# Kernel tuning notes

Measured on AMD Instinct MI355X. Metric: run time of the kernel, lower is better.

The kernel has to match this reference:

```python
import jax, jax.numpy as jnp
import numpy as np

B, L, H = 4, 1024, 8192
NH, HD = 64, 128
PD = HD // 2  # 64, rope-style positional dim
QL = HD * 4 * 3  # 1536, Q latent dim
KVL = HD * 4     # 512, KV latent dim


def setup_inputs() -> dict:
    key = jax.random.key(0)
    ks = jax.random.split(key, 18)
    w = lambda k, i, o: (jax.random.normal(k, (i, o), jnp.float32) * (1.0 / np.sqrt(i))).astype(jnp.float32)
    b = lambda k, o: jnp.zeros((o,), jnp.float32)
    return {
        'x': jax.random.normal(ks[0], (B, L, H), jnp.float32),
        'W_dq': w(ks[1], H, QL),   'b_dq': b(ks[2], QL),
        'W_dkv': w(ks[3], H, KVL), 'b_dkv': b(ks[4], KVL),
        'W_uq': w(ks[5], QL, H),   'b_uq': b(ks[6], H),
        'W_uk': w(ks[7], KVL, H),  'b_uk': b(ks[8], H),
        'W_uv': w(ks[9], KVL, H),  'b_uv': b(ks[10], H),
        'W_pq': w(ks[11], QL, NH * PD), 'b_pq': b(ks[12], NH * PD),
        'W_pk': w(ks[13], H, PD),  'b_pk': b(ks[14], PD),
        'W_o': w(ks[15], H, H),    'b_o': b(ks[16], H),
    }


def reference(x, W_dq, b_dq, W_dkv, b_dkv, W_uq, b_uq, W_uk, b_uk,
              W_uv, b_uv, W_pq, b_pq, W_pk, b_pk, W_o, b_o):
    Bb, Ll, Hh = x.shape
    # low-rank latents
    Q_lat = x @ W_dq + b_dq          # (B, L, 1536)
    KV_lat = x @ W_dkv + b_dkv       # (B, L, 512)
    # up-projections
    Q_c = (Q_lat @ W_uq + b_uq).reshape(Bb, Ll, NH, HD)
    Q_r = (Q_lat @ W_pq + b_pq).reshape(Bb, Ll, NH, PD)
    Q = jnp.concatenate([Q_c, Q_r], axis=-1)            # (B, L, NH, 192)
    K_c = (KV_lat @ W_uk + b_uk).reshape(Bb, Ll, NH, HD)
    K_r = x @ W_pk + b_pk                                # (B, L, 64), shared across heads
    K_r = jnp.broadcast_to(K_r[:, :, None, :], (Bb, Ll, NH, PD))
    K = jnp.concatenate([K_c, K_r], axis=-1)             # (B, L, NH, 192)
    V = (KV_lat @ W_uv + b_uv).reshape(Bb, Ll, NH, HD)   # (B, L, NH, 128)
    # attention with mismatched Q/K (192) vs V (128) head dims; scale by sqrt(128)
    scores = jnp.einsum('bqhd,bkhd->bhqk', Q, K) / np.float32(np.sqrt(HD))
    causal = jnp.tril(jnp.ones((Ll, Ll), bool))
    scores = jnp.where(causal, scores, jnp.float32(-jnp.inf))
    attn = jax.nn.softmax(scores, axis=-1)               # dropout = identity (eval)
    out = jnp.einsum('bhqk,bkhd->bqhd', attn, V).reshape(Bb, Ll, Hh)
    return out @ W_o + b_o
```

## Files before the change

### kernel.cpp

```cpp
#include <hip/hip_runtime.h>
#include <cstdint>

typedef unsigned short u16;
typedef __attribute__((ext_vector_type(8))) short bf16x8;
typedef __attribute__((ext_vector_type(4))) float f32x4;
typedef __attribute__((ext_vector_type(4))) unsigned short u16x4;

__device__ __forceinline__ u16 f2b(float f) {
  union { float f; uint32_t u; } v; v.f = f;
  uint32_t r = v.u + 0x7FFFu + ((v.u >> 16) & 1u);
  return (u16)(r >> 16);
}

__device__ __forceinline__ void gload_lds16(const void* g, void* l) {
  __builtin_amdgcn_global_load_lds((const __attribute__((address_space(1))) void*)g,
                                   (__attribute__((address_space(3))) void*)l, 16, 0, 0);
}

__device__ __forceinline__ void barrier_raw() {
  __builtin_amdgcn_sched_barrier(0);
  asm volatile("" ::: "memory");
  __builtin_amdgcn_s_barrier();
  asm volatile("" ::: "memory");
  __builtin_amdgcn_sched_barrier(0);
}
__device__ __forceinline__ void wait_vm8() {
  asm volatile("s_waitcnt vmcnt(8)" ::: "memory");
  __builtin_amdgcn_sched_barrier(0);
}

__global__ __launch_bounds__(256) void cvt_bf16(const float* __restrict__ in,
                                                u16* __restrict__ out, long n) {
  long i = ((long)blockIdx.x * 256 + threadIdx.x) * 4;
  if (i >= n) return;
  f32x4 v = *(const f32x4*)(in + i);
  u16x4 o;
#pragma unroll
  for (int k = 0; k < 4; k++) o[k] = f2b(v[k]);
  *(u16x4*)(out + i) = o;
}

__global__ __launch_bounds__(256) void transpose_cvt(const float* __restrict__ W,
                                                     u16* __restrict__ WT, int K, int N) {
  __shared__ float tile[32][33];
  const int tn0 = blockIdx.x * 32;
  const int tk0 = blockIdx.y * 32;
  const int c = threadIdx.x & 31;
  const int r0 = threadIdx.x >> 5;
#pragma unroll
  for (int rr = 0; rr < 32; rr += 8)
    tile[r0 + rr][c] = W[(long)(tk0 + r0 + rr) * N + tn0 + c];
  __syncthreads();
#pragma unroll
  for (int rr = 0; rr < 32; rr += 8)
    WT[(long)(tn0 + r0 + rr) * K + tk0 + c] = f2b(tile[c][r0 + rr]);
}

__global__ __launch_bounds__(256) void biascat3(const float* __restrict__ a,
                                                const float* __restrict__ b,
                                                const float* __restrict__ c,
                                                float* __restrict__ o) {
  int i = blockIdx.x * 256 + threadIdx.x;
  if (i < 1536) o[i] = a[i];
  else if (i < 2048) o[i] = b[i - 1536];
  else if (i < 2112) o[i] = c[i - 2048];
}
__global__ __launch_bounds__(256) void biascat2(const float* __restrict__ a,
                                                const float* __restrict__ b,
                                                int na, int n, float* __restrict__ o) {
  int i = blockIdx.x * 256 + threadIdx.x;
  if (i >= n) return;
  o[i] = (i < na) ? a[i] : b[i - na];
}

__global__ __launch_bounds__(256) void repl_kr(const u16* __restrict__ Kr,
                                               u16* __restrict__ Kbuf, int stride) {
  long idx = (long)blockIdx.x * 256 + threadIdx.x;
  int d4 = idx & 15;
  long t = idx >> 4;
  int hh = t & 63;
  long tok = t >> 6;
  if (tok >= 4096) return;
  u16x4 v = *(const u16x4*)(Kr + tok * (long)stride + d4 * 4);
  long b = tok >> 10, l = tok & 1023;
  *(u16x4*)(Kbuf + ((b * 64 + hh) * 1024 + l) * 192 + 128 + d4 * 4) = v;
}

template<int MODE>
__global__ __launch_bounds__(512, 2) void gemm256(
    const u16* __restrict__ A, long lda, const u16* __restrict__ BT,
    const float* __restrict__ bias, void* __restrict__ outp, void* __restrict__ outp2,
    int N, int K) {
  __shared__ u16 sA[2][2][8192];
  __shared__ u16 sB[2][2][8192];
  const int tid = threadIdx.x;
  const int lane = tid & 63;
  const int w = tid >> 6;
  const int wr = w >> 2, wc = w & 3;
  const int hi = lane >> 4, lo = lane & 15;

  const int Nt = gridDim.x, Mt = gridDim.y;
  const int bid = blockIdx.y * Nt + blockIdx.x;
  const int xcd = bid & 7;
  const int idx = bid >> 3;
  int mt, nt;
  if ((Nt & 1) == 0) {
    const int Rm = Mt >> 2, Rn = Nt >> 1;
    const int xr = xcd & 3, xcn = xcd >> 2;
    const int Wb = Rn < 8 ? Rn : 8;
    const int cb = idx / (Rm * Wb);
    const int rem = idx - cb * (Rm * Wb);
    mt = xr * Rm + (rem % Rm);
    nt = xcn * Rn + cb * Wb + rem / Rm;
  } else {
    const int Rm = Mt >> 3;
    const int Wb = Nt < 8 ? Nt : 8;
    const int cb = idx / (Rm * Wb);
    const int rem = idx - cb * (Rm * Wb);
    mt = xcd * Rm + (rem % Rm);
    nt = cb * Wb + rem / Rm;
  }
  const long m0 = (long)mt * 256;
  const long n0 = (long)nt * 256;

  const int nkt = K >> 6;

  const int srow = tid >> 2;
  const int scol = ((tid & 3) ^ ((tid >> 3) & 3)) * 8;
  const long arow0 = m0 + srow, arow1 = arow0 + 128;
  long brow0 = n0 + srow, brow1 = brow0 + 128;
  if (brow0 > N - 1) brow0 = N - 1;
  if (brow1 > N - 1) brow1 = N - 1;
  const u16* aS0 = A + arow0 * lda + scol;
  const u16* aS1 = A + arow1 * lda + scol;
  const u16* bS0 = BT + brow0 * (long)K + scol;
  const u16* bS1 = BT + brow1 * (long)K + scol;

  const int aRd = (wr * 128 + lo) * 32 + (hi ^ ((lo >> 1) & 3)) * 8;
  const int bRd = (wc * 64 + lo) * 32 + (hi ^ ((lo >> 1) & 3)) * 8;

  f32x4 acc[8][4] = {};

#define STAGE(s0, s1, koff, dst) do { \
    gload_lds16((s0) + (koff), (dst) + tid * 8); \
    gload_lds16((s1) + (koff), (dst) + 4096 + tid * 8); \
  } while (0)
#define LDA_F(bufr, kh, m) (*(const bf16x8*)(&sA[bufr][kh][aRd + (m) * 512]))
#define LDB_F(bufr, kh, n) (*(const bf16x8*)(&sB[bufr][kh][bRd + (n) * 512]))
#define MFMA_GRP(mi, av) \
    acc[mi][0] = __builtin_amdgcn_mfma_f32_16x16x32_bf16(av, b0, acc[mi][0], 0, 0, 0); \
    acc[mi][1] = __builtin_amdgcn_mfma_f32_16x16x32_bf16(av, b1, acc[mi][1], 0, 0, 0); \
    acc[mi][2] = __builtin_amdgcn_mfma_f32_16x16x32_bf16(av, b2, acc[mi][2], 0, 0, 0); \
    acc[mi][3] = __builtin_amdgcn_mfma_f32_16x16x32_bf16(av, b3, acc[mi][3], 0, 0, 0);

  STAGE(aS0, aS1, 0, &sA[0][0][0]);
  STAGE(bS0, bS1, 0, &sB[0][0][0]);
  STAGE(aS0, aS1, 32, &sA[0][1][0]);
  STAGE(bS0, bS1, 32, &sB[0][1][0]);
  {
    const long t1o = (nkt > 1) ? 64 : 0;
    STAGE(aS0, aS1, t1o, &sA[1][0][0]);
    STAGE(bS0, bS1, t1o, &sB[1][0][0]);
  }
  wait_vm8();
  barrier_raw();

  for (int t = 0; t < nkt; ++t) {
    const int cur = t & 1, nxt = cur ^ 1;
    const int t1c = (t + 1 < nkt) ? t + 1 : nkt - 1;
    const int t2c = (t + 2 < nkt) ? t + 2 : nkt - 1;
    const long o1 = (long)t1c * 64;
    const long o2 = (long)t2c * 64;
    bf16x8 b0, b1, b2, b3, a0, a1, a2, a3, a4, a5, a6, a7;
    b0 = LDB_F(cur, 0, 0); b1 = LDB_F(cur, 0, 1); b2 = LDB_F(cur, 0, 2); b3 = LDB_F(cur, 0, 3);
    a0 = LDA_F(cur, 0, 0); a1 = LDA_F(cur, 0, 1); a2 = LDA_F(cur, 0, 2); a3 = LDA_F(cur, 0, 3);
    a4 = LDA_F(cur, 0, 4); a5 = LDA_F(cur, 0, 5); a6 = LDA_F(cur, 0, 6); a7 = LDA_F(cur, 0, 7);
    STAGE(aS0, aS1, o1 + 32, &sA[nxt][1][0]);
    barrier_raw();
    __builtin_amdgcn_s_setprio(1);
    MFMA_GRP(0, a0) MFMA_GRP(1, a1) MFMA_GRP(2, a2) MFMA_GRP(3, a3)
    __builtin_amdgcn_s_setprio(0);
    STAGE(bS0, bS1, o1 + 32, &sB[nxt][1][0]);
    __builtin_amdgcn_s_setprio(1);
    MFMA_GRP(4, a4) MFMA_GRP(5, a5) MFMA_GRP(6, a6) MFMA_GRP(7, a7)
    __builtin_amdgcn_s_setprio(0);
    wait_vm8();
    barrier_raw();
    b0 = LDB_F(cur, 1, 0); b1 = LDB_F(cur, 1, 1); b2 = LDB_F(cur, 1, 2); b3 = LDB_F(cur, 1, 3);
    a0 = LDA_F(cur, 1, 0); a1 = LDA_F(cur, 1, 1); a2 = LDA_F(cur, 1, 2); a3 = LDA_F(cur, 1, 3);
    a4 = LDA_F(cur, 1, 4); a5 = LDA_F(cur, 1, 5); a6 = LDA_F(cur, 1, 6); a7 = LDA_F(cur, 1, 7);
    STAGE(aS0, aS1, o2, &sA[cur][0][0]);
    barrier_raw();
    __builtin_amdgcn_s_setprio(1);
    MFMA_GRP(0, a0) MFMA_GRP(1, a1) MFMA_GRP(2, a2) MFMA_GRP(3, a3)
    __builtin_amdgcn_s_setprio(0);
    STAGE(bS0, bS1, o2, &sB[cur][0][0]);
    __builtin_amdgcn_s_setprio(1);
    MFMA_GRP(4, a4) MFMA_GRP(5, a5) MFMA_GRP(6, a6) MFMA_GRP(7, a7)
    __builtin_amdgcn_s_setprio(0);
    wait_vm8();
    barrier_raw();
  }
  asm volatile("s_waitcnt vmcnt(0)" ::: "memory");

#undef STAGE
#undef LDA_F
#undef LDB_F
#undef MFMA_GRP

#pragma unroll
  for (int m = 0; m < 8; m++) {
#pragma unroll
    for (int n = 0; n < 4; n++) {
      const long mb = m0 + wr * 128 + m * 16 + hi * 4;
      const long nn = n0 + wc * 64 + n * 16 + lo;
      if (nn >= N) continue;
      const float bv = bias[nn];
      if (MODE == 0) {
#pragma unroll
        for (int r = 0; r < 4; r++)
          ((u16*)outp)[(mb + r) * (long)N + nn] = f2b(acc[m][n][r] + bv);
      } else if (MODE == 3) {
#pragma unroll
        for (int r = 0; r < 4; r++)
          ((float*)outp)[(mb + r) * (long)N + nn] = acc[m][n][r] + bv;
      } else if (MODE == 4) {
        if (nn < 8192) {
          const long h = nn >> 7, d = nn & 127;
#pragma unroll
          for (int r = 0; r < 4; r++) {
            const long mm = mb + r;
            const long bq = mm >> 10, l = mm & 1023;
            ((u16*)outp)[((bq * 64 + h) * 1024 + l) * 192 + d] = f2b(acc[m][n][r] + bv);
          }
        } else {
          const long q = nn - 8192;
          const long h = q >> 6, d = q & 63;
#pragma unroll
          for (int r = 0; r < 4; r++) {
            const long mm = mb + r;
            const long bq = mm >> 10, l = mm & 1023;
            ((u16*)outp)[((bq * 64 + h) * 1024 + l) * 192 + 128 + d] = f2b(acc[m][n][r] + bv);
          }
        }
      } else {
        if (nn < 8192) {
          const long h = nn >> 7, d = nn & 127;
#pragma unroll
          for (int r = 0; r < 4; r++) {
            const long mm = mb + r;
            const long bq = mm >> 10, l = mm & 1023;
            ((u16*)outp)[((bq * 64 + h) * 1024 + l) * 192 + d] = f2b(acc[m][n][r] + bv);
          }
        } else {
          const long v = nn - 8192;
          const long h = v >> 7, d = v & 127;
          u16x4 pk;
#pragma unroll
          for (int r = 0; r < 4; r++) pk[r] = f2b(acc[m][n][r] + bv);
          const long bq = mb >> 10, l = mb & 1023;
          *(u16x4*)((u16*)outp2 + ((bq * 64 + h) * 128 + d) * 1024 + l) = pk;
        }
      }
    }
  }
}

__global__ __launch_bounds__(512, 2) void attn256(const u16* __restrict__ Qb,
                                                  const u16* __restrict__ Kb,
                                                  const u16* __restrict__ Vt,
                                                  u16* __restrict__ O) {
  __shared__ u16 sK[2][12288];
  __shared__ u16 sV[2][8192];
  __shared__ u16 P[8][32][72];
  const int bh = blockIdx.x;
  const int qtb = 3 - blockIdx.y;
  const int b = bh >> 6, h = bh & 63;
  const int tid = threadIdx.x, w = tid >> 6, lane = tid & 63;
  const int hi = lane >> 4, lo = lane & 15, lo7 = lane & 7;
  const int q0w = qtb * 256 + w * 32;
  const u16* Qh = Qb + (size_t)bh * 1024 * 192;
  const u16* Kh = Kb + (size_t)bh * 1024 * 192;
  const u16* Vh = Vt + (size_t)bh * 128 * 1024;
  const float scale = 0.08838834764831845f;
  const float NEGINF = -3.0e38f;

  int kOff0, kOff1, kOff2, vOff0, vOff1;
  {
    int g0 = tid, g1 = tid + 512, g2 = tid + 1024;
    int r0 = g0 / 24, r1 = g1 / 24, r2 = g2 / 24;
    kOff0 = r0 * 192 + ((g0 - r0 * 24) ^ (r0 & 7)) * 8;
    kOff1 = r1 * 192 + ((g1 - r1 * 24) ^ (r1 & 7)) * 8;
    kOff2 = r2 * 192 + ((g2 - r2 * 24) ^ (r2 & 7)) * 8;
    int s0 = tid, s1 = tid + 512;
    vOff0 = (s0 >> 3) * 1024 + ((s0 & 7) ^ ((s0 >> 3) & 7)) * 8;
    vOff1 = (s1 >> 3) * 1024 + ((s1 & 7) ^ ((s1 >> 3) & 7)) * 8;
  }
#define STAGE_KV(tt, bb) do { \
    const u16* kb_ = Kh + (size_t)(tt) * (64 * 192); \
    const u16* vb_ = Vh + (size_t)(tt) * 64; \
    gload_lds16(kb_ + kOff0, &sK[bb][0] + tid * 8); \
    gload_lds16(kb_ + kOff1, &sK[bb][4096] + tid * 8); \
    gload_lds16(kb_ + kOff2, &sK[bb][8192] + tid * 8); \
    gload_lds16(vb_ + vOff0, &sV[bb][0] + tid * 8); \
    gload_lds16(vb_ + vOff1, &sV[bb][4096] + tid * 8); \
  } while (0)

  bf16x8 qf[2][6];
#pragma unroll
  for (int qi = 0; qi < 2; qi++) {
    const u16* qp = Qh + (size_t)(q0w + qi * 16 + lo) * 192 + hi * 8;
#pragma unroll
    for (int f = 0; f < 6; f++) qf[qi][f] = *(const bf16x8*)(qp + f * 32);
  }

  f32x4 oacc[2][8] = {};
  float m_run[2][4], l_run[2][4];
#pragma unroll
  for (int qi = 0; qi < 2; qi++)
#pragma unroll
    for (int r = 0; r < 4; r++) { m_run[qi][r] = NEGINF; l_run[qi][r] = 0.f; }

  const int nkt = (qtb + 1) * 4;
  STAGE_KV(0, 0);
  __syncthreads();

  for (int t = 0; t < nkt; t++) {
    const int cur = t & 1;
    const int tn = (t + 1 < nkt) ? t + 1 : nkt - 1;
    STAGE_KV(tn, cur ^ 1);
    const int k0 = t * 64;
    if (k0 < q0w + 32) {
      f32x4 s[2][4] = {};
      __builtin_amdgcn_s_setprio(1);
#pragma unroll
      for (int j = 0; j < 4; j++) {
#pragma unroll
        for (int f = 0; f < 6; f++) {
          bf16x8 kf = *(const bf16x8*)(&sK[cur][((j * 16 + lo) * 24 + ((f * 4 + hi) ^ lo7)) * 8]);
          s[0][j] = __builtin_amdgcn_mfma_f32_16x16x32_bf16(qf[0][f], kf, s[0][j], 0, 0, 0);
          s[1][j] = __builtin_amdgcn_mfma_f32_16x16x32_bf16(qf[1][f], kf, s[1][j], 0, 0, 0);
        }
      }
      __builtin_amdgcn_s_setprio(0);
      const bool diag = (k0 + 63 > q0w);
#pragma unroll
      for (int qi = 0; qi < 2; qi++) {
#pragma unroll
        for (int r = 0; r < 4; r++) {
          const int q = q0w + qi * 16 + hi * 4 + r;
          float sv[4];
          float mx = NEGINF;
#pragma unroll
          for (int j = 0; j < 4; j++) {
            float v = s[qi][j][r] * scale;
            if (diag && (k0 + j * 16 + lo > q)) v = NEGINF;
            sv[j] = v;
            mx = fmaxf(mx, v);
          }
#pragma unroll
          for (int o = 1; o < 16; o <<= 1) mx = fmaxf(mx, __shfl_xor(mx, o, 64));
          const float mnew = fmaxf(m_run[qi][r], mx);
          float sum = 0.f;
#pragma unroll
          for (int j = 0; j < 4; j++) {
            float pv = __expf(sv[j] - mnew);
            sum += pv;
            P[w][qi * 16 + hi * 4 + r][j * 16 + lo] = f2b(pv);
          }
#pragma unroll
          for (int o = 1; o < 16; o <<= 1) sum += __shfl_xor(sum, o, 64);
          const float alpha = __expf(m_run[qi][r] - mnew);
          l_run[qi][r] = l_run[qi][r] * alpha + sum;
          m_run[qi][r] = mnew;
#pragma unroll
          for (int j = 0; j < 8; j++) oacc[qi][j][r] *= alpha;
        }
      }
      __builtin_amdgcn_s_setprio(1);
#pragma unroll
      for (int kk = 0; kk < 2; kk++) {
        bf16x8 pf0 = *(const bf16x8*)(&P[w][lo][kk * 32 + hi * 8]);
        bf16x8 pf1 = *(const bf16x8*)(&P[w][16 + lo][kk * 32 + hi * 8]);
#pragma unroll
        for (int j = 0; j < 8; j++) {
          bf16x8 vf = *(const bf16x8*)(&sV[cur][((j * 16 + lo) * 8 + ((kk * 4 + hi) ^ lo7)) * 8]);
          oacc[0][j] = __builtin_amdgcn_mfma_f32_16x16x32_bf16(pf0, vf, oacc[0][j], 0, 0, 0);
          oacc[1][j] = __builtin_amdgcn_mfma_f32_16x16x32_bf16(pf1, vf, oacc[1][j], 0, 0, 0);
        }
      }
      __builtin_amdgcn_s_setprio(0);
    }
    __syncthreads();
  }
#undef STAGE_KV

#pragma unroll
  for (int qi = 0; qi < 2; qi++) {
#pragma unroll
    for (int r = 0; r < 4; r++) {
      const float inv = 1.f / l_run[qi][r];
      const int q = q0w + qi * 16 + hi * 4 + r;
      u16* op = O + ((size_t)(b * 1024 + q) * 64 + h) * 128;
#pragma unroll
      for (int j = 0; j < 8; j++)
        op[j * 16 + lo] = f2b(oacc[qi][j][r] * inv);
    }
  }
}

extern "C" void kernel_launch(void* const* d_in, const int* in_sizes, int n_in,
                              void* d_out, int out_size, void* d_ws, size_t ws_size,
                              hipStream_t stream) {
  const float* x     = (const float*)d_in[0];
  const float* W_dq  = (const float*)d_in[1];
  const float* b_dq  = (const float*)d_in[2];
  const float* W_dkv = (const float*)d_in[3];
  const float* b_dkv = (const float*)d_in[4];
  const float* W_uq  = (const float*)d_in[5];
  const float* b_uq  = (const float*)d_in[6];
  const float* W_uk  = (const float*)d_in[7];
  const float* b_uk  = (const float*)d_in[8];
  const float* W_uv  = (const float*)d_in[9];
  const float* b_uv  = (const float*)d_in[10];
  const float* W_pq  = (const float*)d_in[11];
  const float* b_pq  = (const float*)d_in[12];
  const float* W_pk  = (const float*)d_in[13];
  const float* b_pk  = (const float*)d_in[14];
  const float* W_o   = (const float*)d_in[15];
  const float* b_o   = (const float*)d_in[16];

  char* ws = (char*)d_ws;
  size_t off = 0;
  auto alloc = [&](size_t bytes) {
    char* p = ws + off;
    off += (bytes + 255) & ~(size_t)255;
    return p;
  };
  u16* xbf   = (u16*)alloc(33554432ULL * 2);
  u16* WT    = (u16*)alloc(67108864ULL * 2);
  u16* lat   = (u16*)alloc(4096ULL * 2112 * 2);
  float* bct = (float*)alloc(2112ULL * 4);
  float* bq  = (float*)alloc(12288ULL * 4);
  float* bkv = (float*)alloc(16384ULL * 4);
  u16* Qbuf  = (u16*)alloc(100663296ULL);
  u16* Kbuf  = (u16*)alloc(100663296ULL);
  u16* Vt    = (u16*)alloc(67108864ULL);
  u16* Obuf  = xbf;
  if (off > ws_size) return;

  dim3 blk(256), blk5(512);
  cvt_bf16<<<dim3(32768), blk, 0, stream>>>(x, xbf, 33554432L);
  transpose_cvt<<<dim3(48, 256), blk, 0, stream>>>(W_dq, WT, 8192, 1536);
  transpose_cvt<<<dim3(16, 256), blk, 0, stream>>>(W_dkv, WT + 1536L * 8192, 8192, 512);
  transpose_cvt<<<dim3(2, 256), blk, 0, stream>>>(W_pk, WT + 2048L * 8192, 8192, 64);
  biascat3<<<dim3(9), blk, 0, stream>>>(b_dq, b_dkv, b_pk, bct);
  gemm256<0><<<dim3(9, 16), blk5, 0, stream>>>(xbf, 8192, WT, bct, lat, nullptr, 2112, 8192);
  repl_kr<<<dim3(16384), blk, 0, stream>>>(lat + 2048, Kbuf, 2112);
  transpose_cvt<<<dim3(256, 48), blk, 0, stream>>>(W_uq, WT, 1536, 8192);
  transpose_cvt<<<dim3(128, 48), blk, 0, stream>>>(W_pq, WT + 8192L * 1536, 1536, 4096);
  biascat2<<<dim3(48), blk, 0, stream>>>(b_uq, b_pq, 8192, 12288, bq);
  gemm256<4><<<dim3(48, 16), blk5, 0, stream>>>(lat, 2112, WT, bq, Qbuf, nullptr, 12288, 1536);
  transpose_cvt<<<dim3(256, 16), blk, 0, stream>>>(W_uk, WT, 512, 8192);
  transpose_cvt<<<dim3(256, 16), blk, 0, stream>>>(W_uv, WT + 8192L * 512, 512, 8192);
  biascat2<<<dim3(64), blk, 0, stream>>>(b_uk, b_uv, 8192, 16384, bkv);
  gemm256<5><<<dim3(64, 16), blk5, 0, stream>>>(lat + 1536, 2112, WT, bkv, Kbuf, Vt, 16384, 512);
  attn256<<<dim3(256, 4), blk5, 0, stream>>>(Qbuf, Kbuf, Vt, Obuf);
  transpose_cvt<<<dim3(256, 256), blk, 0, stream>>>(W_o, WT, 8192, 8192);
  gemm256<3><<<dim3(32, 16), blk5, 0, stream>>>(Obuf, 8192, WT, b_o, d_out, nullptr, 8192, 8192);
}
```

Measured before the change: 1.381 ms.

## Split-K the latent down-projection GEMM with a combine kernel

The first GEMM (4096x2112, K=8192) launched only 144 workgroups on a device with many more CUs. The K dimension is now split into four slices along blockIdx.z, each writing fp32 partial sums into scratch space that aliases Qbuf. A new kernel then sums the partials, adds the bias and converts to bf16. This trades an extra round of fp32 writes and reads (about 138 MB each way) for four times more workgroups to raise CU utilisation.

```diff
diff --git a/kernel.cpp b/kernel.cpp
--- a/kernel.cpp
+++ b/kernel.cpp
@@ -71,6 +71,23 @@
   int i = blockIdx.x * 256 + threadIdx.x;
   if (i >= n) return;
   o[i] = (i < na) ? a[i] : b[i - na];
+}
+
+__global__ __launch_bounds__(256) void latcombine(const float* __restrict__ p,
+                                                  const float* __restrict__ bias,
+                                                  u16* __restrict__ lat) {
+  const long S = 4096L * 2112;
+  long i = ((long)blockIdx.x * 256 + threadIdx.x) * 4;
+  if (i >= S) return;
+  f32x4 s0 = *(const f32x4*)(p + i);
+  f32x4 s1 = *(const f32x4*)(p + S + i);
+  f32x4 s2 = *(const f32x4*)(p + 2 * S + i);
+  f32x4 s3 = *(const f32x4*)(p + 3 * S + i);
+  const int n = (int)(i % 2112);
+  u16x4 o;
+#pragma unroll
+  for (int k = 0; k < 4; k++) o[k] = f2b(s0[k] + s1[k] + s2[k] + s3[k] + bias[n + k]);
+  *(u16x4*)(lat + i) = o;
 }
 
 __global__ __launch_bounds__(256) void repl_kr(const u16* __restrict__ Kr,
@@ -88,7 +105,7 @@
 
 template<int MODE>
 __global__ __launch_bounds__(512, 2) void gemm256(
-    const u16* __restrict__ A, long lda, const u16* __restrict__ BT,
+    const u16* __restrict__ A, long lda, const u16* __restrict__ BT, long ldb,
     const float* __restrict__ bias, void* __restrict__ outp, void* __restrict__ outp2,
     int N, int K) {
   __shared__ u16 sA[2][2][8192];
@@ -124,6 +141,7 @@
   const long n0 = (long)nt * 256;
 
   const int nkt = K >> 6;
+  const long kb = (long)blockIdx.z * K;
 
   const int srow = tid >> 2;
   const int scol = ((tid & 3) ^ ((tid >> 3) & 3)) * 8;
@@ -131,10 +149,10 @@
   long brow0 = n0 + srow, brow1 = brow0 + 128;
   if (brow0 > N - 1) brow0 = N - 1;
   if (brow1 > N - 1) brow1 = N - 1;
-  const u16* aS0 = A + arow0 * lda + scol;
-  const u16* aS1 = A + arow1 * lda + scol;
-  const u16* bS0 = BT + brow0 * (long)K + scol;
-  const u16* bS1 = BT + brow1 * (long)K + scol;
+  const u16* aS0 = A + arow0 * lda + kb + scol;
+  const u16* aS1 = A + arow1 * lda + kb + scol;
+  const u16* bS0 = BT + brow0 * ldb + kb + scol;
+  const u16* bS1 = BT + brow1 * ldb + kb + scol;
 
   const int aRd = (wr * 128 + lo) * 32 + (hi ^ ((lo >> 1) & 3)) * 8;
   const int bRd = (wc * 64 + lo) * 32 + (hi ^ ((lo >> 1) & 3)) * 8;
@@ -224,6 +242,11 @@
 #pragma unroll
         for (int r = 0; r < 4; r++)
           ((float*)outp)[(mb + r) * (long)N + nn] = acc[m][n][r] + bv;
+      } else if (MODE == 6) {
+        float* po = (float*)outp + (size_t)blockIdx.z * (4096ULL * 2112ULL);
+#pragma unroll
+        for (int r = 0; r < 4; r++)
+          po[(mb + r) * (long)N + nn] = acc[m][n][r];
       } else if (MODE == 4) {
         if (nn < 8192) {
           const long h = nn >> 7, d = nn & 127;
@@ -447,6 +470,7 @@
   u16* Kbuf  = (u16*)alloc(100663296ULL);
   u16* Vt    = (u16*)alloc(67108864ULL);
   u16* Obuf  = xbf;
+  float* pf  = (float*)Qbuf;
   if (off > ws_size) return;
 
   dim3 blk(256), blk5(512);
@@ -455,17 +479,18 @@
   transpose_cvt<<<dim3(16, 256), blk, 0, stream>>>(W_dkv, WT + 1536L * 8192, 8192, 512);
   transpose_cvt<<<dim3(2, 256), blk, 0, stream>>>(W_pk, WT + 2048L * 8192, 8192, 64);
   biascat3<<<dim3(9), blk, 0, stream>>>(b_dq, b_dkv, b_pk, bct);
-  gemm256<0><<<dim3(9, 16), blk5, 0, stream>>>(xbf, 8192, WT, bct, lat, nullptr, 2112, 8192);
+  gemm256<6><<<dim3(9, 16, 4), blk5, 0, stream>>>(xbf, 8192, WT, 8192, bct, pf, nullptr, 2112, 2048);
+  latcombine<<<dim3(8448), blk, 0, stream>>>(pf, bct, lat);
   repl_kr<<<dim3(16384), blk, 0, stream>>>(lat + 2048, Kbuf, 2112);
   transpose_cvt<<<dim3(256, 48), blk, 0, stream>>>(W_uq, WT, 1536, 8192);
   transpose_cvt<<<dim3(128, 48), blk, 0, stream>>>(W_pq, WT + 8192L * 1536, 1536, 4096);
   biascat2<<<dim3(48), blk, 0, stream>>>(b_uq, b_pq, 8192, 12288, bq);
-  gemm256<4><<<dim3(48, 16), blk5, 0, stream>>>(lat, 2112, WT, bq, Qbuf, nullptr, 12288, 1536);
+  gemm256<4><<<dim3(48, 16), blk5, 0, stream>>>(lat, 2112, WT, 1536, bq, Qbuf, nullptr, 12288, 1536);
   transpose_cvt<<<dim3(256, 16), blk, 0, stream>>>(W_uk, WT, 512, 8192);
   transpose_cvt<<<dim3(256, 16), blk, 0, stream>>>(W_uv, WT + 8192L * 512, 512, 8192);
   biascat2<<<dim3(64), blk, 0, stream>>>(b_uk, b_uv, 8192, 16384, bkv);
-  gemm256<5><<<dim3(64, 16), blk5, 0, stream>>>(lat + 1536, 2112, WT, bkv, Kbuf, Vt, 16384, 512);
+  gemm256<5><<<dim3(64, 16), blk5, 0, stream>>>(lat + 1536, 2112, WT, 512, bkv, Kbuf, Vt, 16384, 512);
   attn256<<<dim3(256, 4), blk5, 0, stream>>>(Qbuf, Kbuf, Vt, Obuf);
   transpose_cvt<<<dim3(256, 256), blk, 0, stream>>>(W_o, WT, 8192, 8192);
-  gemm256<3><<<dim3(32, 16), blk5, 0, stream>>>(Obuf, 8192, WT, b_o, d_out, nullptr, 8192, 8192);
-}
+  gemm256<3><<<dim3(32, 16), blk5, 0, stream>>>(Obuf, 8192, WT, 8192, b_o, d_out, nullptr, 8192, 8192);
+}
```

Measured after the change: 1.383 ms. No clear change (+0.2%).
